# Optimization experiments

Hardware: AMD Instinct MI355X
Metric: run time of the kernel (lower is better)

## Reference

```python
import jax, jax.numpy as jnp
import numpy as np

NHEAD, TOKEN_DIM, HIDDEN, OUT_DIM = 4, 768, 256, 768
B, L = 16, 1024
EPS = 1e-5
SLOPE = 0.01  # default LeakyReLU negative_slope


def _layernorm(x, g, b):
    mu = jnp.mean(x, axis=-1, keepdims=True)
    var = jnp.var(x, axis=-1, keepdims=True)
    return (x - mu) * jax.lax.rsqrt(var + EPS) * g + b


def setup_inputs() -> dict:
    key = jax.random.key(0)
    ks = jax.random.split(key, 8)
    s = 0.02
    return {
        "token_embedding": jax.random.normal(ks[0], (B, L, TOKEN_DIM), jnp.float32),
        "W_fc": jax.random.normal(ks[1], (NHEAD, TOKEN_DIM, HIDDEN), jnp.float32) * s,
        "b_fc": jnp.zeros((NHEAD, HIDDEN), jnp.float32),
        "ln_g": jnp.ones((NHEAD, HIDDEN), jnp.float32),
        "ln_b": jnp.zeros((NHEAD, HIDDEN), jnp.float32),
        "a_w": jax.random.normal(ks[2], (NHEAD, 2 * HIDDEN), jnp.float32) * s,
        "a_b": jnp.zeros((NHEAD,), jnp.float32),
        "W_cat": jax.random.normal(ks[3], (NHEAD * HIDDEN, OUT_DIM), jnp.float32) * s,
        "b_cat": jnp.zeros((OUT_DIM,), jnp.float32),
        "lnO_g": jnp.ones((OUT_DIM,), jnp.float32),
        "lnO_b": jnp.zeros((OUT_DIM,), jnp.float32),
        "W_fcs": jax.random.normal(ks[4], (3, OUT_DIM, OUT_DIM), jnp.float32) * s,
        "b_fcs": jnp.zeros((3, OUT_DIM), jnp.float32),
    }


def reference(token_embedding, W_fc, b_fc, ln_g, ln_b, a_w, a_b,
              W_cat, b_cat, lnO_g, lnO_b, W_fcs, b_fcs):
    # per-head projection + layernorm: h [n, B, L, H]
    h = jnp.einsum('bld,ndh->nblh', token_embedding, W_fc) + b_fc[:, None, None, :]
    h = _layernorm(h, ln_g[:, None, None, :], ln_b[:, None, None, :])
    # attn_fc(concat[h_j, h_i]) decomposes linearly:
    # score[n,b,i,j] = a1 . h[n,b,j] + a2 . h[n,b,i] + bias
    s_row = jnp.einsum('nblh,nh->nbl', h, a_w[:, :HIDDEN])   # varies with j
    s_col = jnp.einsum('nblh,nh->nbl', h, a_w[:, HIDDEN:])   # varies with i
    e = s_col[:, :, :, None] + s_row[:, :, None, :] + a_b[:, None, None, None]
    e = jnp.where(e >= 0, e, SLOPE * e)  # LeakyReLU
    attn = jax.nn.softmax(e, axis=-1)    # softmax over j
    h_prime = jnp.einsum('nbij,nbjh->nbih', attn, h)  # [n, B, L, H]
    # concat heads on feature dim -> [B, L, n*H]
    concat_out = jnp.transpose(h_prime, (1, 2, 0, 3)).reshape(B, L, NHEAD * HIDDEN)
    sent = jnp.mean(concat_out, axis=1)  # [B, n*H]
    sent = sent @ W_cat + b_cat
    sent = _layernorm(sent, lnO_g, lnO_b)
    dims_out = [sent @ W_fcs[i] + b_fcs[i] for i in range(3)]
    return (dims_out[0], dims_out[1], dims_out[2], sent)
```

## Files before the change

kernel.cpp:

```cpp
#include <hip/hip_runtime.h>
#include <math.h>


#define NH   4
#define TD   768
#define HID  256
#define OD   768
#define BB   16
#define LL   1024
#define RTOT (BB*LL)

typedef __attribute__((ext_vector_type(8))) short bf16x8;
typedef __attribute__((ext_vector_type(4))) float f32x4;

__device__ __forceinline__ float lrelu(float x) { return fmaxf(x, 0.01f * x); }

__device__ __forceinline__ float waveReduceSum(float v) {
  #pragma unroll
  for (int m = 1; m < 64; m <<= 1) v += __shfl_xor(v, m, 64);
  return v;
}
__device__ __forceinline__ float waveReduceMax(float v) {
  #pragma unroll
  for (int m = 1; m < 64; m <<= 1) v = fmaxf(v, __shfl_xor(v, m, 64));
  return v;
}
__device__ __forceinline__ float red16(float v) {
  v += __shfl_xor(v, 1, 64); v += __shfl_xor(v, 2, 64);
  v += __shfl_xor(v, 4, 64); v += __shfl_xor(v, 8, 64);
  return v;
}

__device__ __forceinline__ unsigned short f2b(float f) {
  union { float f; unsigned u; } v; v.f = f;
  unsigned u = v.u;
  return (unsigned short)((u + 0x7fffu + ((u >> 16) & 1u)) >> 16);
}
__device__ __forceinline__ float b2f(unsigned short h) {
  union { unsigned u; float f; } v; v.u = ((unsigned)h) << 16;
  return v.f;
}

__device__ __forceinline__ void gll16(const void* g, void* l) {
  __builtin_amdgcn_global_load_lds(
      (const __attribute__((address_space(1))) unsigned int*)g,
      (__attribute__((address_space(3))) unsigned int*)l, 16, 0, 0);
}

__global__ __launch_bounds__(256) void kconv(const float* __restrict__ T,
                                             const float* __restrict__ Wfc,
                                             unsigned short* __restrict__ Tb,
                                             unsigned short* __restrict__ Wtb) {
  __shared__ float tile[64][65];
  const int t = threadIdx.x;
  if (blockIdx.x < 6144) {
    const size_t i = ((size_t)blockIdx.x * 256 + t) * 8;
    const float4 a = *(const float4*)(T + i);
    const float4 b = *(const float4*)(T + i + 4);
    bf16x8 o;
    o[0] = (short)f2b(a.x); o[1] = (short)f2b(a.y);
    o[2] = (short)f2b(a.z); o[3] = (short)f2b(a.w);
    o[4] = (short)f2b(b.x); o[5] = (short)f2b(b.y);
    o[6] = (short)f2b(b.z); o[7] = (short)f2b(b.w);
    *(bf16x8*)(Tb + i) = o;
  } else {
    const int b2 = blockIdx.x - 6144;
    const int ct = b2 & 3;
    const int kt = (b2 >> 2) % 12;
    const int n  = b2 / 48;
    #pragma unroll
    for (int i = 0; i < 16; ++i) {
      const int kl = i * 4 + (t >> 6), cl = t & 63;
      tile[kl][cl] =
          Wfc[(size_t)n * TD * HID + (size_t)(kt * 64 + kl) * HID + ct * 64 + cl];
    }
    __syncthreads();
    #pragma unroll
    for (int i = 0; i < 16; ++i) {
      const int cl = i * 4 + (t >> 6), kl = t & 63;
      Wtb[(size_t)n * HID * TD + (size_t)(ct * 64 + cl) * TD + kt * 64 + kl] =
          f2b(tile[kl][cl]);
    }
  }
}

__global__ __launch_bounds__(512, 2) void k1_mfma(
    const unsigned short* __restrict__ Tb,
    const unsigned short* __restrict__ Wtb,
    const float* __restrict__ bfc, const float* __restrict__ lng,
    const float* __restrict__ lnb, const float* __restrict__ aw,
    unsigned short* __restrict__ hb,
    float* __restrict__ sR, float* __restrict__ sC)
{
  const int n    = blockIdx.x >> 6;
  const int mb   = blockIdx.x & 63;
  const int t    = threadIdx.x;
  const int lane = t & 63;
  const int wq   = __builtin_amdgcn_readfirstlane(t >> 6);
  const int wm   = wq >> 2;
  const int wn   = wq & 3;
  const int cl   = lane & 15;
  const int rg   = lane >> 4;
  const int row0 = mb * 256;

  __shared__ __align__(16) char smem[131072];

  f32x4 acc[8][4];
  #pragma unroll
  for (int mi = 0; mi < 8; ++mi)
    #pragma unroll
    for (int ni = 0; ni < 4; ++ni) acc[mi][ni] = (f32x4){0.f, 0.f, 0.f, 0.f};

  const char* Tg = (const char*)Tb;
  const char* Wg = (const char*)(Wtb + (size_t)n * HID * TD);

  #define STAGE_A(slot, k0)                                                    \
    do {                                                                       \
      char* base_ = smem + (slot) * 32768;                                     \
      _Pragma("unroll")                                                        \
      for (int i_ = 0; i_ < 2; ++i_) {                                         \
        const int off_ = i_ * 8192 + t * 16;                                   \
        const int r_ = off_ >> 6, kb_ = off_ & 63;                             \
        const int kbs_ = kb_ ^ ((r_ & 3) << 4);                                \
        gll16(Tg + ((size_t)(row0 + r_) * TD + (k0)) * 2 + kbs_, base_ + off_);\
      }                                                                        \
    } while (0)
  #define STAGE_B(slot, k0)                                                    \
    do {                                                                       \
      char* base_ = smem + (slot) * 32768 + 16384;                             \
      _Pragma("unroll")                                                        \
      for (int i_ = 0; i_ < 2; ++i_) {                                         \
        const int off_ = i_ * 8192 + t * 16;                                   \
        const int c_ = off_ >> 6, kb_ = off_ & 63;                             \
        const int kbs_ = kb_ ^ ((c_ & 3) << 4);                                \
        gll16(Wg + ((size_t)c_ * TD + (k0)) * 2 + kbs_, base_ + off_);         \
      }                                                                        \
    } while (0)

  STAGE_A(0, 0);  STAGE_B(0, 0);
  STAGE_A(1, 32); STAGE_B(1, 32);

  const int kk2 = rg * 16;

  #pragma unroll 4
  for (int kt = 0; kt < 24; ++kt) {
    const int slot = kt & 3;
    if (kt < 23) asm volatile("s_waitcnt vmcnt(4)" ::: "memory");
    else         asm volatile("s_waitcnt vmcnt(0)" ::: "memory");
    asm volatile("s_barrier" ::: "memory");

    const char* As = smem + slot * 32768;
    const char* Bs = As + 16384;

    bf16x8 bv[4];
    {
      bf16x8 av[4];
      #pragma unroll
      for (int mi = 0; mi < 4; ++mi) {
        const int row = wm * 128 + mi * 16 + cl;
        av[mi] = *(const bf16x8*)(As + row * 64 + (kk2 ^ ((row & 3) << 4)));
      }
      #pragma unroll
      for (int ni = 0; ni < 4; ++ni) {
        const int row = wn * 64 + ni * 16 + cl;
        bv[ni] = *(const bf16x8*)(Bs + row * 64 + (kk2 ^ ((row & 3) << 4)));
      }
      if (kt < 22) STAGE_A((kt + 2) & 3, (kt + 2) * 32);
      asm volatile("s_waitcnt lgkmcnt(0)" ::: "memory");
      __builtin_amdgcn_sched_barrier(0);
      __builtin_amdgcn_s_setprio(1);
      #pragma unroll
      for (int mi = 0; mi < 4; ++mi)
        #pragma unroll
        for (int ni = 0; ni < 4; ++ni)
          acc[mi][ni] = __builtin_amdgcn_mfma_f32_16x16x32_bf16(
              av[mi], bv[ni], acc[mi][ni], 0, 0, 0);
      __builtin_amdgcn_s_setprio(0);
    }
    asm volatile("s_barrier" ::: "memory");
    {
      bf16x8 av[4];
      #pragma unroll
      for (int mi = 0; mi < 4; ++mi) {
        const int row = wm * 128 + (mi + 4) * 16 + cl;
        av[mi] = *(const bf16x8*)(As + row * 64 + (kk2 ^ ((row & 3) << 4)));
      }
      if (kt < 22) STAGE_B((kt + 2) & 3, (kt + 2) * 32);
      asm volatile("s_waitcnt lgkmcnt(0)" ::: "memory");
      __builtin_amdgcn_sched_barrier(0);
      __builtin_amdgcn_s_setprio(1);
      #pragma unroll
      for (int mi = 0; mi < 4; ++mi)
        #pragma unroll
        for (int ni = 0; ni < 4; ++ni)
          acc[mi + 4][ni] = __builtin_amdgcn_mfma_f32_16x16x32_bf16(
              av[mi], bv[ni], acc[mi + 4][ni], 0, 0, 0);
      __builtin_amdgcn_s_setprio(0);
    }
  }
  #undef STAGE_A
  #undef STAGE_B

  __syncthreads();

  float* redS  = (float*)smem;
  float* redS2 = (float*)(smem + 4096);
  float* redP  = (float*)(smem + 8192);
  float* redC  = (float*)(smem + 12288);
  unsigned short* hs = (unsigned short*)(smem + 16384);

  float bfn[4], gvn[4], bvn[4], a1n[4], a2n[4];
  #pragma unroll
  for (int ni = 0; ni < 4; ++ni) {
    const int c = wn * 64 + ni * 16 + cl;
    bfn[ni] = bfc[n * HID + c];
    gvn[ni] = lng[n * HID + c];
    bvn[ni] = lnb[n * HID + c];
    a1n[ni] = aw[n * (2 * HID) + c];
    a2n[ni] = aw[n * (2 * HID) + HID + c];
  }

  #pragma unroll
  for (int mi = 0; mi < 8; ++mi) {
    #pragma unroll
    for (int r = 0; r < 4; ++r) {
      float s = 0.f, s2 = 0.f;
      #pragma unroll
      for (int ni = 0; ni < 4; ++ni) {
        const float x = acc[mi][ni][r] + bfn[ni];
        acc[mi][ni][r] = x;
        s += x; s2 += x * x;
      }
      s = red16(s); s2 = red16(s2);
      if (cl == 0) {
        const int lr = wm * 128 + mi * 16 + rg * 4 + r;
        redS [lr * 4 + wn] = s;
        redS2[lr * 4 + wn] = s2;
      }
    }
  }
  __syncthreads();

  #pragma unroll
  for (int mi = 0; mi < 8; ++mi) {
    #pragma unroll
    for (int r = 0; r < 4; ++r) {
      const int lr = wm * 128 + mi * 16 + rg * 4 + r;
      const f32x4 sv  = *(const f32x4*)&redS [lr * 4];
      const f32x4 s2v = *(const f32x4*)&redS2[lr * 4];
      const float st  = sv.x + sv.y + sv.z + sv.w;
      const float s2t = s2v.x + s2v.y + s2v.z + s2v.w;
      const float mu  = st * (1.f / HID);
      const float var = s2t * (1.f / HID) - mu * mu;
      const float rs  = rsqrtf(var + 1e-5f);
      float pr = 0.f, pc = 0.f;
      #pragma unroll
      for (int ni = 0; ni < 4; ++ni) {
        const float hv = (acc[mi][ni][r] - mu) * rs * gvn[ni] + bvn[ni];
        acc[mi][ni][r] = hv;
        pr += hv * a1n[ni]; pc += hv * a2n[ni];
      }
      pr = red16(pr); pc = red16(pc);
      if (cl == 0) { redP[lr * 4 + wn] = pr; redC[lr * 4 + wn] = pc; }
    }
  }
  __syncthreads();
  if (t < 256) {
    const f32x4 pv = *(const f32x4*)&redP[t * 4];
    const f32x4 cv = *(const f32x4*)&redC[t * 4];
    sR[n * RTOT + row0 + t] = pv.x + pv.y + pv.z + pv.w;
    sC[n * RTOT + row0 + t] = cv.x + cv.y + cv.z + cv.w;
  }

  unsigned short* hgb = hb + ((size_t)n * RTOT + row0) * HID;
  #pragma unroll
  for (int s = 0; s < 2; ++s) {
    #pragma unroll
    for (int mi = 0; mi < 4; ++mi)
      #pragma unroll
      for (int r = 0; r < 4; ++r) {
        const int lr = wm * 64 + mi * 16 + rg * 4 + r;
        #pragma unroll
        for (int ni = 0; ni < 4; ++ni)
          hs[lr * 264 + wn * 64 + ni * 16 + cl] = f2b(acc[s * 4 + mi][ni][r]);
      }
    __syncthreads();
    #pragma unroll
    for (int i = 0; i < 8; ++i) {
      const int e  = i * 4096 + t * 8;
      const int lr = e >> 8, cc = e & 255;
      const int g  = (lr >> 6) * 128 + s * 64 + (lr & 63);
      *(bf16x8*)&hgb[(size_t)g * HID + cc] = *(const bf16x8*)&hs[lr * 264 + cc];
    }
    __syncthreads();
  }
}

__global__ __launch_bounds__(256) void k2_lse(
    const float* __restrict__ sR, const float* __restrict__ sC,
    const float* __restrict__ ab, float* __restrict__ q)
{
  const int n  = blockIdx.x >> 7;
  const int b  = (blockIdx.x >> 3) & 15;
  const int ic = blockIdx.x & 7;
  const int t  = threadIdx.x;
  const int base = (n * BB + b) * LL;

  __shared__ float rl[LL];
  __shared__ float red[4];

  const float4 r4 = ((const float4*)(sR + base))[t];
  ((float4*)rl)[t] = r4;
  float tm = fmaxf(fmaxf(r4.x, r4.y), fmaxf(r4.z, r4.w));
  tm = waveReduceMax(tm);
  if ((t & 63) == 0) red[t >> 6] = tm;
  __syncthreads();
  const float rmax = fmaxf(fmaxf(red[0], red[1]), fmaxf(red[2], red[3]));

  const int i  = ic * 128 + (t >> 1);
  const int jh = t & 1;
  const float ci = sC[base + i] + ab[n];
  const float m = lrelu(ci + rmax);
  float z0 = 0.f, z1 = 0.f, z2 = 0.f, z3 = 0.f;
  #pragma unroll 4
  for (int j4 = jh * 128; j4 < jh * 128 + 128; ++j4) {
    const float4 rr = ((const float4*)rl)[j4];
    z0 += __expf(lrelu(ci + rr.x) - m);
    z1 += __expf(lrelu(ci + rr.y) - m);
    z2 += __expf(lrelu(ci + rr.z) - m);
    z3 += __expf(lrelu(ci + rr.w) - m);
  }
  float z = (z0 + z1) + (z2 + z3);
  z += __shfl_xor(z, 1, 64);
  if (!jh) q[base + i] = m + __logf(z);
}

__global__ __launch_bounds__(256) void k23_colw(
    const unsigned short* __restrict__ h, const float* __restrict__ sR,
    const float* __restrict__ sC, const float* __restrict__ ab,
    const float* __restrict__ q, float* __restrict__ partial)
{
  const int n  = blockIdx.x >> 7;
  const int b  = (blockIdx.x >> 3) & 15;
  const int jc = blockIdx.x & 7;
  const int t  = threadIdx.x;
  const int base = (n * BB + b) * LL;

  __shared__ float cls[LL];
  __shared__ float qls[LL];
  __shared__ float wl[128];
  __shared__ float red2[8][256];

  ((float4*)cls)[t] = ((const float4*)(sC + base))[t];
  ((float4*)qls)[t] = ((const float4*)(q + base))[t];
  __syncthreads();

  {
    const int j  = jc * 128 + (t >> 1);
    const int ih = t & 1;
    const float rj = sR[base + j] + ab[n];
    float z0 = 0.f, z1 = 0.f, z2 = 0.f, z3 = 0.f;
    #pragma unroll 4
    for (int i4 = ih * 128; i4 < ih * 128 + 128; ++i4) {
      const float4 cc = ((const float4*)cls)[i4];
      const float4 qq = ((const float4*)qls)[i4];
      z0 += __expf(lrelu(cc.x + rj) - qq.x);
      z1 += __expf(lrelu(cc.y + rj) - qq.y);
      z2 += __expf(lrelu(cc.z + rj) - qq.z);
      z3 += __expf(lrelu(cc.w + rj) - qq.w);
    }
    float z = (z0 + z1) + (z2 + z3);
    z += __shfl_xor(z, 1, 64);
    if (!ih) wl[t >> 1] = z * (1.f / LL);
  }
  __syncthreads();

  const int jl = t >> 5;
  const int cg = t & 31;
  const unsigned short* hp =
      h + ((size_t)n * RTOT + b * LL + jc * 128) * HID + cg * 8;
  float a0=0,a1=0,a2=0,a3=0,a4=0,a5=0,a6=0,a7=0;
  #pragma unroll 4
  for (int j = jl; j < 128; j += 8) {
    const bf16x8 v = *(const bf16x8*)(hp + (size_t)j * HID);
    const float w = wl[j];
    a0 = fmaf(w, b2f((unsigned short)v[0]), a0);
    a1 = fmaf(w, b2f((unsigned short)v[1]), a1);
    a2 = fmaf(w, b2f((unsigned short)v[2]), a2);
    a3 = fmaf(w, b2f((unsigned short)v[3]), a3);
    a4 = fmaf(w, b2f((unsigned short)v[4]), a4);
    a5 = fmaf(w, b2f((unsigned short)v[5]), a5);
    a6 = fmaf(w, b2f((unsigned short)v[6]), a6);
    a7 = fmaf(w, b2f((unsigned short)v[7]), a7);
  }
  red2[jl][cg*8+0]=a0; red2[jl][cg*8+1]=a1; red2[jl][cg*8+2]=a2; red2[jl][cg*8+3]=a3;
  red2[jl][cg*8+4]=a4; red2[jl][cg*8+5]=a5; red2[jl][cg*8+6]=a6; red2[jl][cg*8+7]=a7;
  __syncthreads();
  float s = 0.f;
  #pragma unroll
  for (int r = 0; r < 8; ++r) s += red2[r][t];
  partial[((n * BB + b) * 8 + jc) * 256 + t] = s;
}

__global__ __launch_bounds__(256) void k4_cat(
    const float* __restrict__ partial, const float* __restrict__ Wcat,
    float* __restrict__ pcat)
{
  const int kc = blockIdx.x / 3;
  const int oc = blockIdx.x % 3;
  const int t  = threadIdx.x;
  __shared__ float s[64][16];
  {
    const int kk = t >> 2, b4 = (t & 3) * 4;
    const int n = kc >> 2;
    const int c = (kc & 3) * 64 + kk;
    #pragma unroll
    for (int bi = 0; bi < 4; ++bi) {
      const int b = b4 + bi;
      const float* pb = partial + (size_t)((n * BB + b) * 8) * 256 + c;
      float v = 0.f;
      #pragma unroll
      for (int j = 0; j < 8; ++j) v += pb[j * 256];
      s[kk][b] = v;
    }
  }
  __syncthreads();
  const int o = oc * 256 + t;
  const float* W = Wcat + (size_t)(kc * 64) * OD + o;
  float acc[BB];
  #pragma unroll
  for (int b = 0; b < BB; ++b) acc[b] = 0.f;
  #pragma unroll 4
  for (int kk = 0; kk < 64; ++kk) {
    const float w = W[(size_t)kk * OD];
    const f32x4 s0 = *(const f32x4*)&s[kk][0];
    const f32x4 s1 = *(const f32x4*)&s[kk][4];
    const f32x4 s2 = *(const f32x4*)&s[kk][8];
    const f32x4 s3 = *(const f32x4*)&s[kk][12];
    acc[0]=fmaf(s0.x,w,acc[0]);  acc[1]=fmaf(s0.y,w,acc[1]);
    acc[2]=fmaf(s0.z,w,acc[2]);  acc[3]=fmaf(s0.w,w,acc[3]);
    acc[4]=fmaf(s1.x,w,acc[4]);  acc[5]=fmaf(s1.y,w,acc[5]);
    acc[6]=fmaf(s1.z,w,acc[6]);  acc[7]=fmaf(s1.w,w,acc[7]);
    acc[8]=fmaf(s2.x,w,acc[8]);  acc[9]=fmaf(s2.y,w,acc[9]);
    acc[10]=fmaf(s2.z,w,acc[10]); acc[11]=fmaf(s2.w,w,acc[11]);
    acc[12]=fmaf(s3.x,w,acc[12]); acc[13]=fmaf(s3.y,w,acc[13]);
    acc[14]=fmaf(s3.z,w,acc[14]); acc[15]=fmaf(s3.w,w,acc[15]);
  }
  float* P = pcat + (size_t)(kc * BB) * OD + o;
  #pragma unroll
  for (int b = 0; b < BB; ++b) P[(size_t)b * OD] = acc[b];
}

__global__ __launch_bounds__(256) void k4_ln(
    const float* __restrict__ pcat, const float* __restrict__ bcat,
    const float* __restrict__ g, const float* __restrict__ be,
    float* __restrict__ sent, float* __restrict__ out_sent)
{
  const int b = blockIdx.x;
  const int t = threadIdx.x;
  __shared__ float red[4][2];
  float x[3];
  #pragma unroll
  for (int i = 0; i < 3; ++i) {
    const int o = i * 256 + t;
    float v = bcat[o];
    #pragma unroll
    for (int kc = 0; kc < 16; ++kc) v += pcat[(size_t)(kc * BB + b) * OD + o];
    x[i] = v;
  }
  float s  = x[0] + x[1] + x[2];
  float s2 = x[0]*x[0] + x[1]*x[1] + x[2]*x[2];
  s = waveReduceSum(s); s2 = waveReduceSum(s2);
  if ((t & 63) == 0) { red[t >> 6][0] = s; red[t >> 6][1] = s2; }
  __syncthreads();
  s  = red[0][0] + red[1][0] + red[2][0] + red[3][0];
  s2 = red[0][1] + red[1][1] + red[2][1] + red[3][1];
  const float mu  = s * (1.f / OD);
  const float var = s2 * (1.f / OD) - mu * mu;
  const float rs  = rsqrtf(var + 1e-5f);
  #pragma unroll
  for (int i = 0; i < 3; ++i) {
    const int o = i * 256 + t;
    const float y = (x[i] - mu) * rs * g[o] + be[o];
    sent[b * OD + o]     = y;
    out_sent[b * OD + o] = y;
  }
}

__global__ __launch_bounds__(256) void k4_fcs(
    const float* __restrict__ sent, const float* __restrict__ Wfcs,
    float* __restrict__ pfcs)
{
  const int kc = blockIdx.x / 9;
  const int r  = blockIdx.x % 9;
  const int i  = r / 3, oc = r % 3;
  const int t  = threadIdx.x;
  __shared__ float s[64][16];
  {
    const int kk = t >> 2, b4 = (t & 3) * 4;
    #pragma unroll
    for (int bi = 0; bi < 4; ++bi)
      s[kk][b4 + bi] = sent[(b4 + bi) * OD + kc * 64 + kk];
  }
  __syncthreads();
  const int o = oc * 256 + t;
  const float* W = Wfcs + (size_t)i * OD * OD + (size_t)(kc * 64) * OD + o;
  float acc[BB];
  #pragma unroll
  for (int b = 0; b < BB; ++b) acc[b] = 0.f;
  #pragma unroll 4
  for (int kk = 0; kk < 64; ++kk) {
    const float w = W[(size_t)kk * OD];
    const f32x4 s0 = *(const f32x4*)&s[kk][0];
    const f32x4 s1 = *(const f32x4*)&s[kk][4];
    const f32x4 s2 = *(const f32x4*)&s[kk][8];
    const f32x4 s3 = *(const f32x4*)&s[kk][12];
    acc[0]=fmaf(s0.x,w,acc[0]);  acc[1]=fmaf(s0.y,w,acc[1]);
    acc[2]=fmaf(s0.z,w,acc[2]);  acc[3]=fmaf(s0.w,w,acc[3]);
    acc[4]=fmaf(s1.x,w,acc[4]);  acc[5]=fmaf(s1.y,w,acc[5]);
    acc[6]=fmaf(s1.z,w,acc[6]);  acc[7]=fmaf(s1.w,w,acc[7]);
    acc[8]=fmaf(s2.x,w,acc[8]);  acc[9]=fmaf(s2.y,w,acc[9]);
    acc[10]=fmaf(s2.z,w,acc[10]); acc[11]=fmaf(s2.w,w,acc[11]);
    acc[12]=fmaf(s3.x,w,acc[12]); acc[13]=fmaf(s3.y,w,acc[13]);
    acc[14]=fmaf(s3.z,w,acc[14]); acc[15]=fmaf(s3.w,w,acc[15]);
  }
  float* P = pfcs + (size_t)((kc * 3 + i) * BB) * OD + o;
  #pragma unroll
  for (int b = 0; b < BB; ++b) P[(size_t)b * OD] = acc[b];
}

__global__ __launch_bounds__(256) void k4_red(
    const float* __restrict__ pfcs, const float* __restrict__ bfcs,
    float* __restrict__ out)
{
  const int i = blockIdx.x >> 4;
  const int b = blockIdx.x & 15;
  const int t = threadIdx.x;
  #pragma unroll
  for (int oc = 0; oc < 3; ++oc) {
    const int o = oc * 256 + t;
    float v = bfcs[i * OD + o];
    #pragma unroll
    for (int kc = 0; kc < 12; ++kc)
      v += pfcs[(size_t)((kc * 3 + i) * BB + b) * OD + o];
    out[i * (BB * OD) + b * OD + o] = v;
  }
}

extern "C" void kernel_launch(void* const* d_in, const int* in_sizes, int n_in,
                              void* d_out, int out_size, void* d_ws, size_t ws_size,
                              hipStream_t stream)
{
  const float* T    = (const float*)d_in[0];
  const float* Wfc  = (const float*)d_in[1];
  const float* bfc  = (const float*)d_in[2];
  const float* lng  = (const float*)d_in[3];
  const float* lnb  = (const float*)d_in[4];
  const float* aw   = (const float*)d_in[5];
  const float* ab   = (const float*)d_in[6];
  const float* Wcat = (const float*)d_in[7];
  const float* bcat = (const float*)d_in[8];
  const float* lnOg = (const float*)d_in[9];
  const float* lnOb = (const float*)d_in[10];
  const float* Wfcs = (const float*)d_in[11];
  const float* bfcs = (const float*)d_in[12];
  float* out = (float*)d_out;

  char* W = (char*)d_ws;
  unsigned short* Tb  = (unsigned short*)W;
  unsigned short* Wtb = (unsigned short*)(W + 25165824);
  unsigned short* hb  = (unsigned short*)(W + 26738688);
  float* sR      = (float*)(W + 60293120);
  float* sC      = sR + NH * RTOT;
  float* q       = sC + NH * RTOT;
  float* partial = q + NH * RTOT;
  float* sent    = partial + NH * BB * 8 * 256;
  float* pcat    = sent + BB * OD;
  float* pfcs    = pcat + 16 * BB * OD;

  kconv   <<<dim3(6336), dim3(256), 0, stream>>>(T, Wfc, Tb, Wtb);
  k1_mfma <<<dim3(256),  dim3(512), 0, stream>>>(Tb, Wtb, bfc, lng, lnb, aw, hb, sR, sC);
  k2_lse  <<<dim3(512),  dim3(256), 0, stream>>>(sR, sC, ab, q);
  k23_colw<<<dim3(512),  dim3(256), 0, stream>>>(hb, sR, sC, ab, q, partial);
  k4_cat  <<<dim3(48),   dim3(256), 0, stream>>>(partial, Wcat, pcat);
  k4_ln   <<<dim3(16),   dim3(256), 0, stream>>>(pcat, bcat, lnOg, lnOb, sent, out + 3 * BB * OD);
  k4_fcs  <<<dim3(108),  dim3(256), 0, stream>>>(sent, Wfcs, pfcs);
  k4_red  <<<dim3(48),   dim3(256), 0, stream>>>(pfcs, bfcs, out);
}
```

Baseline: 118.4 us.

## Restructure projection GEMM to BK=64 double-buffered pipeline with interleaved warp tiling

```diff
diff --git a/kernel.cpp b/kernel.cpp
--- a/kernel.cpp
+++ b/kernel.cpp
@@ -114,92 +114,110 @@
   const char* Tg = (const char*)Tb;
   const char* Wg = (const char*)(Wtb + (size_t)n * HID * TD);
 
-  #define STAGE_A(slot, k0)                                                    \
+  #define ISSUE_A(Ns, k0, half)                                                \
     do {                                                                       \
-      char* base_ = smem + (slot) * 32768;                                     \
       _Pragma("unroll")                                                        \
-      for (int i_ = 0; i_ < 2; ++i_) {                                         \
-        const int off_ = i_ * 8192 + t * 16;                                   \
-        const int r_ = off_ >> 6, kb_ = off_ & 63;                             \
-        const int kbs_ = kb_ ^ ((r_ & 3) << 4);                                \
-        gll16(Tg + ((size_t)(row0 + r_) * TD + (k0)) * 2 + kbs_, base_ + off_);\
+      for (int j_ = 0; j_ < 2; ++j_) {                                         \
+        const int r_  = (half) * 128 + j_ * 64 + (t >> 3);                     \
+        const int kb_ = (t & 7) * 16;                                          \
+        gll16(Tg + ((size_t)(row0 + r_) * TD + (k0)) * 2 +                     \
+                  (kb_ ^ ((r_ & 7) << 4)),                                     \
+              (Ns) + (half) * 16384 + j_ * 8192 + t * 16);                     \
       }                                                                        \
     } while (0)
-  #define STAGE_B(slot, k0)                                                    \
+  #define ISSUE_B(Ns, k0, half)                                                \
     do {                                                                       \
-      char* base_ = smem + (slot) * 32768 + 16384;                             \
       _Pragma("unroll")                                                        \
-      for (int i_ = 0; i_ < 2; ++i_) {                                         \
-        const int off_ = i_ * 8192 + t * 16;                                   \
-        const int c_ = off_ >> 6, kb_ = off_ & 63;                             \
-        const int kbs_ = kb_ ^ ((c_ & 3) << 4);                                \
-        gll16(Wg + ((size_t)c_ * TD + (k0)) * 2 + kbs_, base_ + off_);         \
+      for (int j_ = 0; j_ < 2; ++j_) {                                         \
+        const int c_  = (half) * 128 + j_ * 64 + (t >> 3);                     \
+        const int kb_ = (t & 7) * 16;                                          \
+        gll16(Wg + ((size_t)c_ * TD + (k0)) * 2 + (kb_ ^ ((c_ & 7) << 4)),     \
+              (Ns) + 32768 + (half) * 16384 + j_ * 8192 + t * 16);             \
       }                                                                        \
     } while (0)
 
-  STAGE_A(0, 0);  STAGE_B(0, 0);
-  STAGE_A(1, 32); STAGE_B(1, 32);
-
-  const int kk2 = rg * 16;
-
-  #pragma unroll 4
-  for (int kt = 0; kt < 24; ++kt) {
-    const int slot = kt & 3;
-    if (kt < 23) asm volatile("s_waitcnt vmcnt(4)" ::: "memory");
-    else         asm volatile("s_waitcnt vmcnt(0)" ::: "memory");
-    asm volatile("s_barrier" ::: "memory");
-
-    const char* As = smem + slot * 32768;
-    const char* Bs = As + 16384;
-
-    bf16x8 bv[4];
+  #define DSR(MH, NH)                                                          \
+    _Pragma("unroll")                                                          \
+    for (int m2 = 0; m2 < 4; ++m2) {                                           \
+      const int r_ = (2 * ((MH) * 4 + m2) + wm) * 16 + cl;                     \
+      _Pragma("unroll")                                                        \
+      for (int ks = 0; ks < 2; ++ks)                                           \
+        av[m2][ks] = *(const bf16x8*)(As + r_ * 128 +                          \
+                         ((ks * 64 + rg * 16) ^ ((r_ & 7) << 4)));             \
+    }                                                                          \
+    _Pragma("unroll")                                                          \
+    for (int n2 = 0; n2 < 2; ++n2) {                                           \
+      const int c_ = (4 * ((NH) * 2 + n2) + wn) * 16 + cl;                     \
+      _Pragma("unroll")                                                        \
+      for (int ks = 0; ks < 2; ++ks)                                           \
+        bv[n2][ks] = *(const bf16x8*)(Bs + c_ * 128 +                          \
+                         ((ks * 64 + rg * 16) ^ ((c_ & 7) << 4)));             \
+    }
+
+  #define MFM(MH, NH)                                                          \
+    __builtin_amdgcn_s_setprio(1);                                             \
+    _Pragma("unroll")                                                          \
+    for (int m2 = 0; m2 < 4; ++m2)                                             \
+      _Pragma("unroll")                                                        \
+      for (int n2 = 0; n2 < 2; ++n2)                                           \
+        _Pragma("unroll")                                                      \
+        for (int ks = 0; ks < 2; ++ks)                                         \
+          acc[(MH) * 4 + m2][(NH) * 2 + n2] =                                  \
+              __builtin_amdgcn_mfma_f32_16x16x32_bf16(                         \
+                  av[m2][ks], bv[n2][ks], acc[(MH) * 4 + m2][(NH) * 2 + n2],   \
+                  0, 0, 0);                                                    \
+    __builtin_amdgcn_s_setprio(0);
+
+  #define VM4 asm volatile("s_waitcnt vmcnt(4)" ::: "memory")
+  #define VM2 asm volatile("s_waitcnt vmcnt(2)" ::: "memory")
+  #define VM0 asm volatile("s_waitcnt vmcnt(0)" ::: "memory")
+  #define BAR asm volatile("s_barrier" ::: "memory")
+  #define PREMFMA                                                              \
+    asm volatile("s_waitcnt lgkmcnt(0)" ::: "memory");                         \
+    __builtin_amdgcn_sched_barrier(0)
+
+  ISSUE_A(smem, 0, 0); ISSUE_B(smem, 0, 0); ISSUE_B(smem, 0, 1); ISSUE_A(smem, 0, 1);
+  VM4; BAR;
+
+  for (int kt = 0; kt < 12; ++kt) {
+    const char* As = smem + (kt & 1) * 65536;
+    const char* Bs = As + 32768;
+    char* Ns = smem + ((kt + 1) & 1) * 65536;
+    const int k1o = (kt + 1) * 64;
+    const bool pf = (kt < 11);
     {
-      bf16x8 av[4];
-      #pragma unroll
-      for (int mi = 0; mi < 4; ++mi) {
-        const int row = wm * 128 + mi * 16 + cl;
-        av[mi] = *(const bf16x8*)(As + row * 64 + (kk2 ^ ((row & 3) << 4)));
-      }
-      #pragma unroll
-      for (int ni = 0; ni < 4; ++ni) {
-        const int row = wn * 64 + ni * 16 + cl;
-        bv[ni] = *(const bf16x8*)(Bs + row * 64 + (kk2 ^ ((row & 3) << 4)));
-      }
-      if (kt < 22) STAGE_A((kt + 2) & 3, (kt + 2) * 32);
-      asm volatile("s_waitcnt lgkmcnt(0)" ::: "memory");
-      __builtin_amdgcn_sched_barrier(0);
-      __builtin_amdgcn_s_setprio(1);
-      #pragma unroll
-      for (int mi = 0; mi < 4; ++mi)
-        #pragma unroll
-        for (int ni = 0; ni < 4; ++ni)
-          acc[mi][ni] = __builtin_amdgcn_mfma_f32_16x16x32_bf16(
-              av[mi], bv[ni], acc[mi][ni], 0, 0, 0);
-      __builtin_amdgcn_s_setprio(0);
-    }
-    asm volatile("s_barrier" ::: "memory");
+      bf16x8 av[4][2], bv[2][2];
+      DSR(0, 0)
+      if (pf) { ISSUE_A(Ns, k1o, 0); VM4; } else { VM2; }
+      BAR; PREMFMA;
+      MFM(0, 0)
+    }
     {
-      bf16x8 av[4];
-      #pragma unroll
-      for (int mi = 0; mi < 4; ++mi) {
-        const int row = wm * 128 + (mi + 4) * 16 + cl;
-        av[mi] = *(const bf16x8*)(As + row * 64 + (kk2 ^ ((row & 3) << 4)));
-      }
-      if (kt < 22) STAGE_B((kt + 2) & 3, (kt + 2) * 32);
-      asm volatile("s_waitcnt lgkmcnt(0)" ::: "memory");
-      __builtin_amdgcn_sched_barrier(0);
-      __builtin_amdgcn_s_setprio(1);
-      #pragma unroll
-      for (int mi = 0; mi < 4; ++mi)
-        #pragma unroll
-        for (int ni = 0; ni < 4; ++ni)
-          acc[mi + 4][ni] = __builtin_amdgcn_mfma_f32_16x16x32_bf16(
-              av[mi], bv[ni], acc[mi + 4][ni], 0, 0, 0);
-      __builtin_amdgcn_s_setprio(0);
-    }
-  }
-  #undef STAGE_A
-  #undef STAGE_B
+      bf16x8 av[4][2], bv[2][2];
+      DSR(0, 1)
+      if (pf) { ISSUE_B(Ns, k1o, 0); VM4; } else { VM0; }
+      BAR; PREMFMA;
+      MFM(0, 1)
+    }
+    {
+      bf16x8 av[4][2], bv[2][2];
+      DSR(1, 0)
+      if (pf) ISSUE_B(Ns, k1o, 1);
+      BAR; PREMFMA;
+      MFM(1, 0)
+    }
+    {
+      bf16x8 av[4][2], bv[2][2];
+      DSR(1, 1)
+      if (pf) { ISSUE_A(Ns, k1o, 1); VM4; }
+      BAR; PREMFMA;
+      MFM(1, 1)
+    }
+  }
+  #undef ISSUE_A
+  #undef ISSUE_B
+  #undef DSR
+  #undef MFM
 
   __syncthreads();
 
@@ -212,7 +230,7 @@
   float bfn[4], gvn[4], bvn[4], a1n[4], a2n[4];
   #pragma unroll
   for (int ni = 0; ni < 4; ++ni) {
-    const int c = wn * 64 + ni * 16 + cl;
+    const int c = (4 * ni + wn) * 16 + cl;
     bfn[ni] = bfc[n * HID + c];
     gvn[ni] = lng[n * HID + c];
     bvn[ni] = lnb[n * HID + c];
@@ -233,7 +251,7 @@
       }
       s = red16(s); s2 = red16(s2);
       if (cl == 0) {
-        const int lr = wm * 128 + mi * 16 + rg * 4 + r;
+        const int lr = (2 * mi + wm) * 16 + rg * 4 + r;
         redS [lr * 4 + wn] = s;
         redS2[lr * 4 + wn] = s2;
       }
@@ -245,7 +263,7 @@
   for (int mi = 0; mi < 8; ++mi) {
     #pragma unroll
     for (int r = 0; r < 4; ++r) {
-      const int lr = wm * 128 + mi * 16 + rg * 4 + r;
+      const int lr = (2 * mi + wm) * 16 + rg * 4 + r;
       const f32x4 sv  = *(const f32x4*)&redS [lr * 4];
       const f32x4 s2v = *(const f32x4*)&redS2[lr * 4];
       const float st  = sv.x + sv.y + sv.z + sv.w;
@@ -274,23 +292,25 @@
 
   unsigned short* hgb = hb + ((size_t)n * RTOT + row0) * HID;
   #pragma unroll
-  for (int s = 0; s < 2; ++s) {
-    #pragma unroll
-    for (int mi = 0; mi < 4; ++mi)
+  for (int c = 0; c < 4; ++c) {
+    #pragma unroll
+    for (int m2 = 0; m2 < 2; ++m2) {
+      const int mi = c * 2 + m2;
       #pragma unroll
       for (int r = 0; r < 4; ++r) {
-        const int lr = wm * 64 + mi * 16 + rg * 4 + r;
+        const int lr = (2 * m2 + wm) * 16 + rg * 4 + r;
         #pragma unroll
         for (int ni = 0; ni < 4; ++ni)
-          hs[lr * 264 + wn * 64 + ni * 16 + cl] = f2b(acc[s * 4 + mi][ni][r]);
+          hs[lr * 264 + (4 * ni + wn) * 16 + cl] = f2b(acc[mi][ni][r]);
       }
+    }
     __syncthreads();
     #pragma unroll
-    for (int i = 0; i < 8; ++i) {
+    for (int i = 0; i < 4; ++i) {
       const int e  = i * 4096 + t * 8;
       const int lr = e >> 8, cc = e & 255;
-      const int g  = (lr >> 6) * 128 + s * 64 + (lr & 63);
-      *(bf16x8*)&hgb[(size_t)g * HID + cc] = *(const bf16x8*)&hs[lr * 264 + cc];
+      *(bf16x8*)&hgb[(size_t)(c * 64 + lr) * HID + cc] =
+          *(const bf16x8*)&hs[lr * 264 + cc];
     }
     __syncthreads();
   }
```

New measurement: 118.1 us. Within noise of the previous version (-0.3%).
